# Performance work log

Hardware: AMD Instinct MI355X
Metric: run time of the kernel (lower is better)

## Reference

```python
import jax, jax.numpy as jnp
import numpy as np

B, LS, LW, LV, M, D, H = 256, 1024, 1024, 1024, 16, 5120, 2048

def setup_inputs() -> dict:
    key = jax.random.key(0)
    ks = jax.random.split(key, 8)
    return {
        'phi_batch': jax.random.normal(ks[0], (B, LS), jnp.float32),
        'w_M_real': jax.random.normal(ks[1], (B, LW, M), jnp.float32),
        'w_M_imag': jax.random.normal(ks[2], (B, LW, M), jnp.float32),
        'v_M': jax.random.normal(ks[3], (LV, M), jnp.float32),
        'W1e': jax.random.normal(ks[4], (D, H), jnp.float32) * 0.02,
        'b1e': jnp.zeros((H,), jnp.float32),
        'W2e': jax.random.normal(ks[5], (H, LS), jnp.float32) * 0.02,
        'b2e': jnp.zeros((LS,), jnp.float32),
        'W1r': jax.random.normal(ks[6], (D, H), jnp.float32) * 0.02,
        'b1r': jnp.zeros((H,), jnp.float32),
        'W2r': jax.random.normal(ks[7], (H, 1), jnp.float32) * 0.02,
        'b2r': jnp.zeros((1,), jnp.float32),
    }

def reference(phi_batch, w_M_real, w_M_imag, v_M, W1e, b1e, W2e, b2e, W1r, b1r, W2r, b2r):
    b, ls = phi_batch.shape
    m = v_M.shape[1]
    # s = (1/sqrt(Ls)) * exp(1j*phi); use real/imag parts directly
    mag = 1.0 / jnp.sqrt(jnp.asarray(ls, jnp.float32))
    s_feat = jnp.concatenate([mag * jnp.cos(phi_batch), mag * jnp.sin(phi_batch)], axis=-1)  # [B, 2Ls]
    # Batched concat across (batch, M): replaces the nested Python loops
    X = jnp.concatenate([
        jnp.broadcast_to(s_feat[:, None, :], (b, m, s_feat.shape[-1])),
        jnp.swapaxes(w_M_real, 1, 2),                       # [B, M, Lw]
        jnp.swapaxes(w_M_imag, 1, 2),                       # [B, M, Lw]
        jnp.broadcast_to(v_M.T[None, :, :], (b, m, v_M.shape[0])),
    ], axis=-1)                                             # [B, M, D]
    eta_M = jax.nn.relu(X @ W1e + b1e) @ W2e + b2e          # [B, M, Ls]
    rho_M = (jax.nn.relu(X @ W1r + b1r) @ W2r + b2r)[..., 0]  # [B, M]
    eta = jnp.einsum('bm,bml->bl', rho_M, eta_M)            # sum_m rho_m * eta_m
    phi_optimal = phi_batch - eta
    return phi_optimal, jnp.swapaxes(eta_M, 1, 2)           # [B, Ls], [B, Ls, M]
```

## Files before the change

### kernel.cpp

```cpp
#include <hip/hip_runtime.h>
#include <hip/hip_bf16.h>
#include <stdint.h>

#define B_    256
#define LS_   1024
#define LW_   1024
#define LV_   1024
#define M_    16
#define D_    5120
#define H_    2048
#define ROWS  4096
#define N1    4096
#define KW    2048

typedef __hip_bfloat16 bf16;
typedef __bf16 bf16x8 __attribute__((ext_vector_type(8)));
typedef __bf16 bf16x4 __attribute__((ext_vector_type(4)));
typedef float f32x4 __attribute__((ext_vector_type(4)));

#define SB0() __builtin_amdgcn_sched_barrier(0)
#define LGKM(n) asm volatile("s_waitcnt lgkmcnt(" #n ")" ::: "memory")
#define VMC(n)  asm volatile("s_waitcnt vmcnt(" #n ")" ::: "memory")

__device__ __forceinline__ void gld_lds16(const void* g, void* l) {
  auto gp = (const __attribute__((address_space(1))) uint32_t*)(uintptr_t)g;
  auto lp = (__attribute__((address_space(3))) uint32_t*)(uint32_t)(uintptr_t)l;
  __builtin_amdgcn_global_load_lds(gp, lp, 16, 0, 0);
}

__device__ __forceinline__ void transpose64_body(char* sm, const float* __restrict__ in,
                                                 bf16* __restrict__ out,
                                                 int C, int R, int r0, int c0, int t) {
  float (*tile)[65] = (float (*)[65])sm;
  const int tx = t & 15, ty = t >> 4;
#pragma unroll
  for (int i = 0; i < 4; ++i) {
    const float4 v = *(const float4*)&in[(size_t)(r0 + ty + i * 16) * C + c0 + tx * 4];
    tile[ty + i * 16][tx * 4 + 0] = v.x;
    tile[ty + i * 16][tx * 4 + 1] = v.y;
    tile[ty + i * 16][tx * 4 + 2] = v.z;
    tile[ty + i * 16][tx * 4 + 3] = v.w;
  }
  __syncthreads();
#pragma unroll
  for (int i = 0; i < 4; ++i) {
    const int n = c0 + ty + i * 16;
    bf16x4 o;
#pragma unroll
    for (int j = 0; j < 4; ++j) o[j] = (__bf16)tile[tx * 4 + j][ty + i * 16];
    *(bf16x4*)&out[(size_t)n * R + r0 + tx * 4] = o;
  }
}

__global__ void __launch_bounds__(256)
prep_kernel(const float* __restrict__ phi,
            const float* __restrict__ wMr, const float* __restrict__ wMi,
            const float* __restrict__ vM,
            const float* __restrict__ W1e, const float* __restrict__ W1r,
            const float* __restrict__ W2e,
            bf16* __restrict__ sfeat, bf16* __restrict__ Awr,
            bf16* __restrict__ W1sT, bf16* __restrict__ W1wT,
            bf16* __restrict__ W2t, float* __restrict__ hVT) {
  __shared__ __align__(16) char sm[32768];
  const int bid = blockIdx.x;
  const int t = threadIdx.x;

  if (bid < 256) {
    float (*vs)[16] = (float (*)[16])sm;
    float (*ws)[16] = (float (*)[16])(sm + 16384);
    const float* Wb = (bid < 128) ? W1e : W1r;
    const int nbase = (bid & 127) * 16;
    const int nout = ((bid < 128) ? 0 : 2048) + nbase;
    const int m = t & 15, nl = t >> 4;
    float acc = 0.f;
    for (int l0 = 0; l0 < 1024; l0 += 256) {
      __syncthreads();
#pragma unroll
      for (int i = 0; i < 16; ++i) {
        int e = i * 256 + t, l = e >> 4, n = e & 15;
        vs[l][n] = vM[(size_t)(l0 + l) * 16 + n];
        ws[l][n] = Wb[(size_t)(4096 + l0 + l) * 2048 + nbase + n];
      }
      __syncthreads();
#pragma unroll 8
      for (int ll = 0; ll < 256; ++ll)
        acc += vs[ll][m] * ws[ll][nl];
    }
    hVT[(size_t)(nout + nl) * 16 + m] = acc;
  } else if (bid < 4352) {
    const int idx = bid - 256;
    const int z = idx >> 10, rem = idx & 1023;
    const float* src = (z == 0 || z == 2) ? W1e : W1r;
    src += (z < 2) ? 0 : (size_t)2048 * 2048;
    bf16* dst = (z < 2) ? W1sT : W1wT;
    dst += (z == 0 || z == 2) ? 0 : (size_t)2048 * 2048;
    transpose64_body(sm, src, dst, 2048, 2048, (rem >> 5) * 64, (rem & 31) * 64, t);
  } else if (bid < 4864) {
    const int idx = bid - 4352;
    transpose64_body(sm, W2e, W2t, LS_, H_, (idx >> 4) * 64, (idx & 15) * 64, t);
  } else if (bid < 8960) {
    const int idx = bid - 4864;
    const int b = idx >> 4, l0 = (idx & 15) * 64;
    float (*tr)[17] = (float (*)[17])sm;
    float (*ti)[17] = (float (*)[17])(sm + 4352 * 4);
    const float* wrb = wMr + (size_t)b * (LW_ * M_) + (size_t)l0 * 16;
    const float* wib = wMi + (size_t)b * (LW_ * M_) + (size_t)l0 * 16;
#pragma unroll
    for (int i = 0; i < 4; ++i) {
      int e = i * 256 + t, l = e >> 4, m = e & 15;
      tr[l][m] = wrb[e];
      ti[l][m] = wib[e];
    }
    __syncthreads();
    int m = t >> 4, t4 = t & 15;
    bf16* outR = Awr + (size_t)(b * 16 + m) * KW + l0;
#pragma unroll
    for (int j = 0; j < 4; ++j) outR[t4 * 4 + j]        = __float2bfloat16(tr[t4 * 4 + j][m]);
#pragma unroll
    for (int j = 0; j < 4; ++j) outR[1024 + t4 * 4 + j] = __float2bfloat16(ti[t4 * 4 + j][m]);
  } else {
    const int i = (bid - 8960) * 256 + t;
    const int b = i >> 10, l = i & 1023;
    float p = phi[i];
    float s, c;
    sincosf(p, &s, &c);
    sfeat[b * 2048 + l]        = __float2bfloat16(0.03125f * c);
    sfeat[b * 2048 + 1024 + l] = __float2bfloat16(0.03125f * s);
  }
}

__global__ void __launch_bounds__(256)
hsum_kernel(const float* __restrict__ hSp, const float* __restrict__ b1e,
            const float* __restrict__ b1r, float* __restrict__ hS2) {
  const int i = (blockIdx.x * 256 + threadIdx.x) * 4;
  const int c = i & (N1 - 1);
  f32x4 v = *(const f32x4*)&hSp[i];
  v = v + *(const f32x4*)&hSp[(size_t)B_ * N1 + i];
  v = v + *(const f32x4*)&hSp[(size_t)2 * B_ * N1 + i];
  v = v + *(const f32x4*)&hSp[(size_t)3 * B_ * N1 + i];
  const float* bp = (c < H_) ? &b1e[c] : &b1r[c - H_];
  v = v + *(const f32x4*)bp;
  *(f32x4*)&hS2[i] = v;
}

__global__ void __launch_bounds__(512, 2)
gemm1_256_kernel(const bf16* __restrict__ A, const bf16* __restrict__ Bt,
                 const float* __restrict__ hS2, const float* __restrict__ hVT,
                 bf16* __restrict__ outH) {
  extern __shared__ __align__(16) char smem[];
  constexpr int NT = KW / 32;

  const int tid  = threadIdx.x;
  const int lane = tid & 63;
  const int wave = tid >> 6;
  const int wr = wave >> 2, wc = wave & 3;
  const int fr = lane & 15, fq = lane >> 4;
  const int row0 = blockIdx.y * 256, col0 = blockIdx.x * 256;

  const int slotF = (((fr & 1) << 2) | fq) ^ ((fr >> 1) & 7);
  const int aOff = (wr << 13) + ((fr >> 1) << 7) + (slotF << 4);
  const int bOff = 16384 + (wc << 12) + ((fr >> 1) << 7) + (slotF << 4);

  const int lg0 = (tid >> 3), lg1 = 64 + (tid >> 3);
  const int su0 = (tid & 7) ^ (lg0 & 7), su1 = (tid & 7) ^ (lg1 & 7);
  const int rowp0 = lg0 * 2 + (su0 >> 2), rowp1 = lg1 * 2 + (su1 >> 2);
  const int kb0 = (su0 & 3) << 4, kb1 = (su1 & 3) << 4;
  const char* pA0 = (const char*)A  + (size_t)(row0 + rowp0) * (KW * 2) + kb0;
  const char* pA1 = (const char*)A  + (size_t)(row0 + rowp1) * (KW * 2) + kb1;
  const char* pB0 = (const char*)Bt + (size_t)(col0 + rowp0) * (KW * 2) + kb0;
  const char* pB1 = (const char*)Bt + (size_t)(col0 + rowp1) * (KW * 2) + kb1;

  auto stageTile = [&](int T) {
    char* dst = smem + (size_t)(T & 3) * 32768;
    const size_t ko = (size_t)T * 64;
    gld_lds16(pA0 + ko, dst + 0     + tid * 16);
    gld_lds16(pA1 + ko, dst + 8192  + tid * 16);
    gld_lds16(pB0 + ko, dst + 16384 + tid * 16);
    gld_lds16(pB1 + ko, dst + 24576 + tid * 16);
  };

  f32x4 acc[8][4] = {};
  bf16x8 bA[4], bB[4];

  stageTile(0); stageTile(1); stageTile(2);
  VMC(4);
  __builtin_amdgcn_s_barrier();
  {
    const char* bP = smem + bOff;
#pragma unroll
    for (int n = 0; n < 4; ++n) bA[n] = *(const bf16x8*)(bP + n * 1024);
  }
  SB0();

  auto doIter = [&](int T, bf16x8 (&bCur)[4], bf16x8 (&bNxt)[4]) {
    const char* aP = smem + (size_t)(T & 3) * 32768 + aOff;
    const char* bP = smem + (size_t)((T + 1) & 3) * 32768 + bOff;
    bf16x8 a[8];
#pragma unroll
    for (int m = 0; m < 4; ++m) a[m] = *(const bf16x8*)(aP + m * 1024);
    SB0();
#pragma unroll
    for (int m = 4; m < 8; ++m) a[m] = *(const bf16x8*)(aP + m * 1024);
    SB0();
#pragma unroll
    for (int n = 0; n < 4; ++n) bNxt[n] = *(const bf16x8*)(bP + n * 1024);
    SB0();
    if (T + 3 < NT) stageTile(T + 3);
    SB0();
    LGKM(8);
    SB0();
    __builtin_amdgcn_s_setprio(1);
#pragma unroll
    for (int m = 0; m < 4; ++m)
#pragma unroll
      for (int n = 0; n < 4; ++n)
        acc[m][n] = __builtin_amdgcn_mfma_f32_16x16x32_bf16(a[m], bCur[n], acc[m][n], 0, 0, 0);
    SB0();
    LGKM(4);
    SB0();
#pragma unroll
    for (int m = 4; m < 8; ++m)
#pragma unroll
      for (int n = 0; n < 4; ++n)
        acc[m][n] = __builtin_amdgcn_mfma_f32_16x16x32_bf16(a[m], bCur[n], acc[m][n], 0, 0, 0);
    __builtin_amdgcn_s_setprio(0);
    SB0();
    LGKM(0);
    if (T + 3 < NT) { VMC(4); }
    else            { VMC(0); }
    __builtin_amdgcn_s_barrier();
  };

  for (int t = 0; t < NT - 2; t += 2) {
    doIter(t,     bA, bB);
    doIter(t + 1, bB, bA);
  }
  doIter(NT - 2, bA, bB);

  {
    const char* aP = smem + (size_t)((NT - 1) & 3) * 32768 + aOff;
    bf16x8 a[8];
#pragma unroll
    for (int m = 0; m < 4; ++m) a[m] = *(const bf16x8*)(aP + m * 1024);
    SB0();
#pragma unroll
    for (int m = 4; m < 8; ++m) a[m] = *(const bf16x8*)(aP + m * 1024);
    SB0();
    LGKM(4);
    SB0();
    __builtin_amdgcn_s_setprio(1);
#pragma unroll
    for (int m = 0; m < 4; ++m)
#pragma unroll
      for (int n = 0; n < 4; ++n)
        acc[m][n] = __builtin_amdgcn_mfma_f32_16x16x32_bf16(a[m], bB[n], acc[m][n], 0, 0, 0);
    SB0();
    LGKM(0);
    SB0();
#pragma unroll
    for (int m = 4; m < 8; ++m)
#pragma unroll
      for (int n = 0; n < 4; ++n)
        acc[m][n] = __builtin_amdgcn_mfma_f32_16x16x32_bf16(a[m], bB[n], acc[m][n], 0, 0, 0);
    __builtin_amdgcn_s_setprio(0);
  }

#pragma unroll
  for (int n = 0; n < 4; ++n) {
    const int c = col0 + wc * 64 + n * 16 + fr;
    const f32x4 hv = *(const f32x4*)&hVT[(size_t)c * 16 + fq * 4];
#pragma unroll
    for (int m = 0; m < 8; ++m) {
      const int rbase = row0 + wr * 128 + m * 16;
      const float hs = hS2[(size_t)(rbase >> 4) * N1 + c];
#pragma unroll
      for (int j = 0; j < 4; ++j) {
        const int r = rbase + fq * 4 + j;
        float v = acc[m][n][j] + hs + hv[j];
        outH[(size_t)r * N1 + c] = __float2bfloat16(v > 0.f ? v : 0.f);
      }
    }
  }
}

template <int EPI, int NT>
__global__ void __launch_bounds__(256, 2)
gemm128_pipe_kernel(const bf16* __restrict__ A, int lda,
                    const bf16* __restrict__ Bt, int ldb,
                    const float* __restrict__ bias0, const float* __restrict__ rho,
                    const float* __restrict__ phi,
                    float* __restrict__ outS, float* __restrict__ out0) {
  extern __shared__ __align__(16) char smem[];

  if (EPI == 1) {
    const int z = blockIdx.z;
    A    += (size_t)z * 512;
    Bt   += (size_t)z * 512;
    outS += (size_t)z * ((size_t)B_ * N1);
  }

  const int tid  = threadIdx.x;
  const int lane = tid & 63;
  const int wave = tid >> 6;
  const int wr = wave >> 1, wc = wave & 1;
  const int fr = lane & 15, fq = lane >> 4;
  const int row0 = blockIdx.y * 128, col0 = blockIdx.x * 128;

  const int slotF = (((fr & 1) << 2) | fq) ^ ((fr >> 1) & 7);
  const int aOff = (wr << 12) + ((fr >> 1) << 7) + (slotF << 4);
  const int bOff = 8192 + (wc << 12) + ((fr >> 1) << 7) + (slotF << 4);

  const int lgl = tid >> 3;
  const int su  = (tid & 7) ^ (lgl & 7);
  const int rp0 = lgl * 2 + (su >> 2);
  const int rp1 = (32 + lgl) * 2 + (su >> 2);
  const int kb  = (su & 3) << 4;
  const char* pA0 = (const char*)A  + (size_t)(row0 + rp0) * ((size_t)lda * 2) + kb;
  const char* pA1 = (const char*)A  + (size_t)(row0 + rp1) * ((size_t)lda * 2) + kb;
  const char* pB0 = (const char*)Bt + (size_t)(col0 + rp0) * ((size_t)ldb * 2) + kb;
  const char* pB1 = (const char*)Bt + (size_t)(col0 + rp1) * ((size_t)ldb * 2) + kb;

  auto stageTile = [&](int T) {
    char* dst = smem + (size_t)(T & 3) * 16384;
    const size_t ko = (size_t)T * 64;
    gld_lds16(pA0 + ko, dst + 0     + tid * 16);
    gld_lds16(pA1 + ko, dst + 4096  + tid * 16);
    gld_lds16(pB0 + ko, dst + 8192  + tid * 16);
    gld_lds16(pB1 + ko, dst + 12288 + tid * 16);
  };

  f32x4 acc[4][4] = {};
  bf16x8 bA[4], bB[4];

  stageTile(0); stageTile(1); stageTile(2);
  VMC(4);
  __builtin_amdgcn_s_barrier();
  {
    const char* bP = smem + bOff;
#pragma unroll
    for (int n = 0; n < 4; ++n) bA[n] = *(const bf16x8*)(bP + n * 1024);
  }
  SB0();

  auto doIter = [&](int T, bf16x8 (&bCur)[4], bf16x8 (&bNxt)[4]) {
    const char* aP = smem + (size_t)(T & 3) * 16384 + aOff;
    const char* bP = smem + (size_t)((T + 1) & 3) * 16384 + bOff;
    bf16x8 a[4];
#pragma unroll
    for (int m = 0; m < 4; ++m) a[m] = *(const bf16x8*)(aP + m * 1024);
    SB0();
#pragma unroll
    for (int n = 0; n < 4; ++n) bNxt[n] = *(const bf16x8*)(bP + n * 1024);
    SB0();
    if (T + 3 < NT) stageTile(T + 3);
    SB0();
    LGKM(4);
    SB0();
    __builtin_amdgcn_s_setprio(1);
#pragma unroll
    for (int m = 0; m < 4; ++m)
#pragma unroll
      for (int n = 0; n < 4; ++n)
        acc[m][n] = __builtin_amdgcn_mfma_f32_16x16x32_bf16(a[m], bCur[n], acc[m][n], 0, 0, 0);
    __builtin_amdgcn_s_setprio(0);
    SB0();
    LGKM(0);
    if (T + 3 < NT) { VMC(4); }
    else            { VMC(0); }
    __builtin_amdgcn_s_barrier();
  };

  for (int t = 0; t < NT - 2; t += 2) {
    doIter(t,     bA, bB);
    doIter(t + 1, bB, bA);
  }
  doIter(NT - 2, bA, bB);

  {
    const char* aP = smem + (size_t)((NT - 1) & 3) * 16384 + aOff;
    bf16x8 a[4];
#pragma unroll
    for (int m = 0; m < 4; ++m) a[m] = *(const bf16x8*)(aP + m * 1024);
    SB0();
    LGKM(0);
    SB0();
    __builtin_amdgcn_s_setprio(1);
#pragma unroll
    for (int m = 0; m < 4; ++m)
#pragma unroll
      for (int n = 0; n < 4; ++n)
        acc[m][n] = __builtin_amdgcn_mfma_f32_16x16x32_bf16(a[m], bB[n], acc[m][n], 0, 0, 0);
    __builtin_amdgcn_s_setprio(0);
  }

  if (EPI == 0) {
#pragma unroll
    for (int m = 0; m < 4; ++m) {
      const int bg = (row0 >> 4) + wr * 4 + m;
      const f32x4 rv = *(const f32x4*)&rho[bg * 16 + fq * 4];
#pragma unroll
      for (int n = 0; n < 4; ++n) {
        const int c = col0 + wc * 64 + n * 16 + fr;
        const float bias = bias0[c];
        float part = 0.f;
#pragma unroll
        for (int j = 0; j < 4; ++j) {
          float v = acc[m][n][j] + bias;
          outS[(size_t)bg * (LS_ * M_) + (size_t)c * M_ + (fq * 4 + j)] = v;
          part += rv[j] * v;
        }
        part += __shfl_xor(part, 16);
        part += __shfl_xor(part, 32);
        if (fq == 0)
          out0[(size_t)bg * LS_ + c] = phi[(size_t)bg * LS_ + c] - part;
      }
    }
  } else {
#pragma unroll
    for (int m = 0; m < 4; ++m) {
#pragma unroll
      for (int n = 0; n < 4; ++n) {
        const int c = col0 + wc * 64 + n * 16 + fr;
#pragma unroll
        for (int j = 0; j < 4; ++j) {
          const int r = row0 + wr * 64 + m * 16 + fq * 4 + j;
          outS[(size_t)r * N1 + c] = acc[m][n][j];
        }
      }
    }
  }
}

__global__ void rho_kernel(const bf16* __restrict__ h, const float* __restrict__ w2r,
                           const float* __restrict__ b2r, float* __restrict__ rho) {
  int r = blockIdx.x;
  int t = threadIdx.x;
  int lane = t & 63, wave = t >> 6;
  const bf16* hr = h + (size_t)r * N1 + H_;
  float s = 0.f;
#pragma unroll
  for (int j = 0; j < 8; ++j)
    s += __bfloat162float(hr[t * 8 + j]) * w2r[t * 8 + j];
#pragma unroll
  for (int off = 32; off > 0; off >>= 1) s += __shfl_down(s, off);
  __shared__ float ws4[4];
  if (lane == 0) ws4[wave] = s;
  __syncthreads();
  if (t == 0) rho[r] = ws4[0] + ws4[1] + ws4[2] + ws4[3] + b2r[0];
}

extern "C" void kernel_launch(void* const* d_in, const int* in_sizes, int n_in,
                              void* d_out, int out_size, void* d_ws, size_t ws_size,
                              hipStream_t stream) {
  const float* phi = (const float*)d_in[0];
  const float* wMr = (const float*)d_in[1];
  const float* wMi = (const float*)d_in[2];
  const float* vM  = (const float*)d_in[3];
  const float* W1e = (const float*)d_in[4];
  const float* b1e = (const float*)d_in[5];
  const float* W2e = (const float*)d_in[6];
  const float* b2e = (const float*)d_in[7];
  const float* W1r = (const float*)d_in[8];
  const float* b1r = (const float*)d_in[9];
  const float* W2r = (const float*)d_in[10];
  const float* b2r = (const float*)d_in[11];

  float* out0 = (float*)d_out;
  float* out1 = out0 + (size_t)B_ * LS_;

  bf16* Awr   = (bf16*)d_ws;
  bf16* W1sT  = Awr  + (size_t)ROWS * KW;
  bf16* W1wT  = W1sT + (size_t)N1 * KW;
  bf16* h     = W1wT + (size_t)N1 * KW;
  bf16* W2t   = h + (size_t)ROWS * N1;
  bf16* sfeat = W2t + (size_t)LS_ * H_;
  float* hSp  = (float*)(sfeat + (size_t)B_ * 2048);
  float* hS2  = hSp + (size_t)4 * B_ * N1;
  float* hVT  = hS2 + (size_t)B_ * N1;
  float* rho  = hVT + (size_t)N1 * 16;

  (void)hipFuncSetAttribute(reinterpret_cast<const void*>(gemm1_256_kernel),
                            hipFuncAttributeMaxDynamicSharedMemorySize, 131072);
  (void)hipFuncSetAttribute(reinterpret_cast<const void*>(gemm128_pipe_kernel<0, 64>),
                            hipFuncAttributeMaxDynamicSharedMemorySize, 65536);
  (void)hipFuncSetAttribute(reinterpret_cast<const void*>(gemm128_pipe_kernel<1, 16>),
                            hipFuncAttributeMaxDynamicSharedMemorySize, 65536);

  prep_kernel<<<9984, 256, 0, stream>>>(phi, wMr, wMi, vM, W1e, W1r, W2e,
                                        sfeat, Awr, W1sT, W1wT, W2t, hVT);

  gemm128_pipe_kernel<1, 16><<<dim3(N1 / 128, B_ / 128, 4), 256, 65536, stream>>>(
      sfeat, 2048, W1sT, KW, nullptr, nullptr, nullptr, hSp, nullptr);

  hsum_kernel<<<(B_ * N1 / 4) / 256, 256, 0, stream>>>(hSp, b1e, b1r, hS2);

  gemm1_256_kernel<<<dim3(N1 / 256, ROWS / 256), 512, 131072, stream>>>(
      Awr, W1wT, hS2, hVT, h);

  rho_kernel<<<ROWS, 256, 0, stream>>>(h, W2r, b2r, rho);

  gemm128_pipe_kernel<0, 64><<<dim3(LS_ / 128, ROWS / 128), 256, 65536, stream>>>(
      h, N1, W2t, H_, b2e, rho, phi, out1, out0);
}
```

Before: 148.7 us.

## Fuse rho head reduction into GEMM1 epilogue and drop rho kernel

The rho head's dot product with W2r is now computed inside the first-layer GEMM epilogue for the rho-half columns. Partial sums are reduced with wave shuffles and shared memory into per-column-block partials, which the final GEMM sums in its prologue. This removes the separate rho kernel launch, stops writing the rho half of h to memory, and avoids re-reading it. It also keeps rho in fp32 instead of rounding it through bf16. In exchange the final GEMM needs a little extra shared memory and a short prologue.

Result: faster. 142.0 us (-4.5%).

```diff
diff --git a/kernel.cpp b/kernel.cpp
--- a/kernel.cpp
+++ b/kernel.cpp
@@ -146,7 +146,8 @@
 __global__ void __launch_bounds__(512, 2)
 gemm1_256_kernel(const bf16* __restrict__ A, const bf16* __restrict__ Bt,
                  const float* __restrict__ hS2, const float* __restrict__ hVT,
-                 bf16* __restrict__ outH) {
+                 const float* __restrict__ w2r,
+                 bf16* __restrict__ outH, float* __restrict__ rhoP) {
   extern __shared__ __align__(16) char smem[];
   constexpr int NT = KW / 32;
 
@@ -265,20 +266,66 @@
     __builtin_amdgcn_s_setprio(0);
   }
 
-#pragma unroll
-  for (int n = 0; n < 4; ++n) {
-    const int c = col0 + wc * 64 + n * 16 + fr;
-    const f32x4 hv = *(const f32x4*)&hVT[(size_t)c * 16 + fq * 4];
+  if (col0 < H_) {
+#pragma unroll
+    for (int n = 0; n < 4; ++n) {
+      const int c = col0 + wc * 64 + n * 16 + fr;
+      const f32x4 hv = *(const f32x4*)&hVT[(size_t)c * 16 + fq * 4];
+#pragma unroll
+      for (int m = 0; m < 8; ++m) {
+        const int rbase = row0 + wr * 128 + m * 16;
+        const float hs = hS2[(size_t)(rbase >> 4) * N1 + c];
+#pragma unroll
+        for (int j = 0; j < 4; ++j) {
+          const int r = rbase + fq * 4 + j;
+          float v = acc[m][n][j] + hs + hv[j];
+          outH[(size_t)r * N1 + c] = __float2bfloat16(v > 0.f ? v : 0.f);
+        }
+      }
+    }
+  } else {
+    const int cb = (col0 >> 8) - 8;
+    float* rhoT = (float*)smem;
+    f32x4 hv4[4];
+    float w2[4];
+#pragma unroll
+    for (int n = 0; n < 4; ++n) {
+      const int c = col0 + wc * 64 + n * 16 + fr;
+      hv4[n] = *(const f32x4*)&hVT[(size_t)c * 16 + fq * 4];
+      w2[n] = w2r[c - H_];
+    }
 #pragma unroll
     for (int m = 0; m < 8; ++m) {
       const int rbase = row0 + wr * 128 + m * 16;
-      const float hs = hS2[(size_t)(rbase >> 4) * N1 + c];
+      const float* hrow = &hS2[(size_t)(rbase >> 4) * N1];
+      f32x4 rsv = {0.f, 0.f, 0.f, 0.f};
+#pragma unroll
+      for (int n = 0; n < 4; ++n) {
+        const int c = col0 + wc * 64 + n * 16 + fr;
+        const float hs = hrow[c];
+#pragma unroll
+        for (int j = 0; j < 4; ++j) {
+          float v = acc[m][n][j] + hs + hv4[n][j];
+          v = v > 0.f ? v : 0.f;
+          rsv[j] += v * w2[n];
+        }
+      }
 #pragma unroll
       for (int j = 0; j < 4; ++j) {
-        const int r = rbase + fq * 4 + j;
-        float v = acc[m][n][j] + hs + hv[j];
-        outH[(size_t)r * N1 + c] = __float2bfloat16(v > 0.f ? v : 0.f);
+        rsv[j] += __shfl_xor(rsv[j], 1);
+        rsv[j] += __shfl_xor(rsv[j], 2);
+        rsv[j] += __shfl_xor(rsv[j], 4);
+        rsv[j] += __shfl_xor(rsv[j], 8);
       }
+      if (fr == 0)
+        *(f32x4*)&rhoT[((wr * 4 + wc) << 7) + m * 16 + fq * 4] = rsv;
+    }
+    __syncthreads();
+    if (tid < 256) {
+      const int wrr = tid >> 7, lr = tid & 127;
+      const float* rt = &rhoT[(wrr * 4) << 7];
+      const float s = rt[lr] + rt[128 + lr] + rt[256 + lr] + rt[384 + lr];
+      rhoP[(size_t)(row0 + wrr * 128 + lr) * 8 + cb] = s;
     }
   }
 }
@@ -287,7 +334,8 @@
 __global__ void __launch_bounds__(256, 2)
 gemm128_pipe_kernel(const bf16* __restrict__ A, int lda,
                     const bf16* __restrict__ Bt, int ldb,
-                    const float* __restrict__ bias0, const float* __restrict__ rho,
+                    const float* __restrict__ bias0,
+                    const float* __restrict__ rhoP, const float* __restrict__ b2r,
                     const float* __restrict__ phi,
                     float* __restrict__ outS, float* __restrict__ out0) {
   extern __shared__ __align__(16) char smem[];
@@ -305,6 +353,19 @@
   const int wr = wave >> 1, wc = wave & 1;
   const int fr = lane & 15, fq = lane >> 4;
   const int row0 = blockIdx.y * 128, col0 = blockIdx.x * 128;
+
+  if (EPI == 0) {
+    if (tid < 128) {
+      const float* pp = &rhoP[(size_t)(row0 + tid) * 8];
+      const f32x4 p0 = *(const f32x4*)pp;
+      const f32x4 p1 = *(const f32x4*)(pp + 4);
+      const float s = p0[0] + p0[1] + p0[2] + p0[3] +
+                      p1[0] + p1[1] + p1[2] + p1[3] + b2r[0];
+      ((float*)(smem + 65536))[tid] = s;
+    }
+    LGKM(0);
+    SB0();
+  }
 
   const int slotF = (((fr & 1) << 2) | fq) ^ ((fr >> 1) & 7);
   const int aOff = (wr << 12) + ((fr >> 1) << 7) + (slotF << 4);
@@ -394,10 +455,11 @@
   }
 
   if (EPI == 0) {
+    const float* rhoL = (const float*)(smem + 65536);
 #pragma unroll
     for (int m = 0; m < 4; ++m) {
       const int bg = (row0 >> 4) + wr * 4 + m;
-      const f32x4 rv = *(const f32x4*)&rho[bg * 16 + fq * 4];
+      const f32x4 rv = *(const f32x4*)&rhoL[wr * 64 + m * 16 + fq * 4];
 #pragma unroll
       for (int n = 0; n < 4; ++n) {
         const int c = col0 + wc * 64 + n * 16 + fr;
@@ -429,24 +491,6 @@
       }
     }
   }
-}
-
-__global__ void rho_kernel(const bf16* __restrict__ h, const float* __restrict__ w2r,
-                           const float* __restrict__ b2r, float* __restrict__ rho) {
-  int r = blockIdx.x;
-  int t = threadIdx.x;
-  int lane = t & 63, wave = t >> 6;
-  const bf16* hr = h + (size_t)r * N1 + H_;
-  float s = 0.f;
-#pragma unroll
-  for (int j = 0; j < 8; ++j)
-    s += __bfloat162float(hr[t * 8 + j]) * w2r[t * 8 + j];
-#pragma unroll
-  for (int off = 32; off > 0; off >>= 1) s += __shfl_down(s, off);
-  __shared__ float ws4[4];
-  if (lane == 0) ws4[wave] = s;
-  __syncthreads();
-  if (t == 0) rho[r] = ws4[0] + ws4[1] + ws4[2] + ws4[3] + b2r[0];
 }
 
 extern "C" void kernel_launch(void* const* d_in, const int* in_sizes, int n_in,
@@ -477,12 +521,12 @@
   float* hSp  = (float*)(sfeat + (size_t)B_ * 2048);
   float* hS2  = hSp + (size_t)4 * B_ * N1;
   float* hVT  = hS2 + (size_t)B_ * N1;
-  float* rho  = hVT + (size_t)N1 * 16;
+  float* rhoP = hVT + (size_t)N1 * 16;
 
   (void)hipFuncSetAttribute(reinterpret_cast<const void*>(gemm1_256_kernel),
                             hipFuncAttributeMaxDynamicSharedMemorySize, 131072);
   (void)hipFuncSetAttribute(reinterpret_cast<const void*>(gemm128_pipe_kernel<0, 64>),
-                            hipFuncAttributeMaxDynamicSharedMemorySize, 65536);
+                            hipFuncAttributeMaxDynamicSharedMemorySize, 66048);
   (void)hipFuncSetAttribute(reinterpret_cast<const void*>(gemm128_pipe_kernel<1, 16>),
                             hipFuncAttributeMaxDynamicSharedMemorySize, 65536);
 
@@ -490,15 +534,13 @@
                                         sfeat, Awr, W1sT, W1wT, W2t, hVT);
 
   gemm128_pipe_kernel<1, 16><<<dim3(N1 / 128, B_ / 128, 4), 256, 65536, stream>>>(
-      sfeat, 2048, W1sT, KW, nullptr, nullptr, nullptr, hSp, nullptr);
+      sfeat, 2048, W1sT, KW, nullptr, nullptr, nullptr, nullptr, hSp, nullptr);
 
   hsum_kernel<<<(B_ * N1 / 4) / 256, 256, 0, stream>>>(hSp, b1e, b1r, hS2);
 
   gemm1_256_kernel<<<dim3(N1 / 256, ROWS / 256), 512, 131072, stream>>>(
-      Awr, W1wT, hS2, hVT, h);
-
-  rho_kernel<<<ROWS, 256, 0, stream>>>(h, W2r, b2r, rho);
-
-  gemm128_pipe_kernel<0, 64><<<dim3(LS_ / 128, ROWS / 128), 256, 65536, stream>>>(
-      h, N1, W2t, H_, b2e, rho, phi, out1, out0);
-}
+      Awr, W1wT, hS2, hVT, W2r, h, rhoP);
+
+  gemm128_pipe_kernel<0, 64><<<dim3(LS_ / 128, ROWS / 128), 256, 66048, stream>>>(
+      h, N1, W2t, H_, b2e, rhoP, b2r, phi, out1, out0);
+}
```
